# Optimization experiments

Hardware: AMD Instinct MI355X
Metric: run time of the kernel (lower is better)

The kernel has to match this reference:

```python
import jax, jax.numpy as jnp
import numpy as np

TOP_K = 2  # router top-k (assumed, standard MoE)


def setup_inputs() -> dict:
    key = jax.random.key(0)
    ks = jax.random.split(key, 8)
    B, T, C, H, E = 4, 1024, 1024, 4096, 8
    s = 0.02
    return {
        "X": jax.random.normal(ks[0], (B, T, C), jnp.float32),
        "router_w": jax.random.normal(ks[1], (C, E), jnp.float32) * s,
        "sh_w1": jax.random.normal(ks[2], (C, H), jnp.float32) * s,
        "sh_b1": jnp.zeros((H,), jnp.float32),
        "sh_w2": jax.random.normal(ks[3], (H, C), jnp.float32) * s,
        "sh_b2": jnp.zeros((C,), jnp.float32),
        "rt_w1": jax.random.normal(ks[4], (E, C, H), jnp.float32) * s,
        "rt_b1": jnp.zeros((E, H), jnp.float32),
        "rt_w2": jax.random.normal(ks[5], (E, H, C), jnp.float32) * s,
        "rt_b2": jnp.zeros((E, C), jnp.float32),
    }


def reference(X, router_w, sh_w1, sh_b1, sh_w2, sh_b2, rt_w1, rt_b1, rt_w2, rt_b2):
    B, T, C = X.shape
    E = router_w.shape[1]

    # --- router: softmax over experts, top-k weights/indices ---
    logits = jnp.einsum("btc,ce->bte", X, router_w)
    probs = jax.nn.softmax(logits, axis=-1)                 # [B,T,E]
    weights, indices = jax.lax.top_k(probs, TOP_K)          # [B,T,K]

    # --- aux load-balance loss: E * sum_i f_i * P_i ---
    onehot = jax.nn.one_hot(indices, E, dtype=X.dtype)      # [B,T,K,E]
    f = onehot.sum(axis=2).mean(axis=(0, 1))                # fraction of tokens per expert
    P = probs.mean(axis=(0, 1))                             # mean router prob per expert
    aux_loss = E * jnp.sum(f * P)

    # --- shared expert(s): single MLP (num_shared_experts = 1) ---
    shared = jnp.einsum("bth,hc->btc", jax.nn.relu(jnp.einsum("btc,ch->bth", X, sh_w1) + sh_b1), sh_w2) + sh_b2

    # --- routed experts: dense all-expert MLP, then weighted combine ---
    h = jax.nn.relu(jnp.einsum("btc,ech->bteh", X, rt_w1) + rt_b1)        # [B,T,E,H]
    y = jnp.einsum("bteh,ehc->btec", h, rt_w2) + rt_b2                    # [B,T,E,C]
    w_full = jnp.einsum("btk,btke->bte", weights, onehot)                 # per-token expert weight
    routed = jnp.einsum("bte,btec->btc", w_full, y)

    return shared + routed, aux_loss
```

## Files before the change

### kernel.cpp

```cpp
#include <hip/hip_runtime.h>


typedef unsigned short u16;
typedef __bf16 bf16x8 __attribute__((ext_vector_type(8)));
typedef float f32x4 __attribute__((ext_vector_type(4)));

#define NTOK 4096
#define CDIM 1024
#define HDIM 4096
#define NEXP 8
#define SLOTS 14336
#define NTILES 56
#define RBLK 1024

#define WAITVM(N) do { asm volatile("s_waitcnt vmcnt(" #N ")" ::: "memory"); } while (0)

static __device__ __forceinline__ u16 f2bf(float f) {
  unsigned u = __float_as_uint(f);
  u += 0x7fffu + ((u >> 16) & 1u);
  return (u16)(u >> 16);
}

static __device__ __forceinline__ void gload16(const void* g, void* l) {
  __builtin_amdgcn_global_load_lds((const __attribute__((address_space(1))) unsigned int*)g,
                                   (__attribute__((address_space(3))) unsigned int*)l,
                                   16, 0, 0);
}

__global__ void init_kernel(int* order, int* tile_expert, int* cursor) {
  int i = blockIdx.x * 256 + threadIdx.x;
  if (i < SLOTS) order[i] = (i < NTOK) ? i : -1;
  if (i < NTILES) tile_expert[i] = (i < 16) ? 8 : -1;
  if (i < NEXP) cursor[i] = 0;
}

__global__ void xconv_kernel(const float* __restrict__ X, u16* __restrict__ Xb) {
  int i = blockIdx.x * 256 + threadIdx.x;
  float4 v = ((const float4*)X)[i];
  u16 o0 = f2bf(v.x), o1 = f2bf(v.y), o2 = f2bf(v.z), o3 = f2bf(v.w);
  unsigned long long pack = (unsigned long long)o0 | ((unsigned long long)o1 << 16)
                          | ((unsigned long long)o2 << 32) | ((unsigned long long)o3 << 48);
  ((unsigned long long*)Xb)[i] = pack;
}

__global__ void tconv_kernel(const float* __restrict__ src, u16* __restrict__ dst, int R, int Cc) {
  __shared__ float t[32][33];
  const size_t bofs = (size_t)blockIdx.z * R * Cc;
  src += bofs; dst += bofs;
  int tx = threadIdx.x & 31, ty = threadIdx.x >> 5;
  int r0 = blockIdx.y * 32, c0 = blockIdx.x * 32;
#pragma unroll
  for (int i = 0; i < 32; i += 8)
    t[ty + i][tx] = src[(size_t)(r0 + ty + i) * Cc + c0 + tx];
  __syncthreads();
#pragma unroll
  for (int i = 0; i < 32; i += 8)
    dst[(size_t)(c0 + ty + i) * R + r0 + tx] = f2bf(t[tx][ty + i]);
}

__global__ __launch_bounds__(256) void router_kernel(
    const float* __restrict__ X, const float* __restrict__ rw,
    float* __restrict__ w01, int* __restrict__ e01,
    float* __restrict__ pP, int* __restrict__ pC) {
  __shared__ float wP[4][8];
  __shared__ int wE[4][2];
  const int tid = threadIdx.x;
  const int w = tid >> 6, l = tid & 63;
  const int wid = blockIdx.x * 4 + w;
  const float* x = X + (size_t)wid * CDIM;
  float s[8] = {0.f,0.f,0.f,0.f,0.f,0.f,0.f,0.f};
#pragma unroll 4
  for (int i = 0; i < 16; ++i) {
    int c = i * 64 + l;
    float xv = x[c];
    const float4* rp = (const float4*)(rw + c * 8);
    float4 r0 = rp[0], r1 = rp[1];
    s[0] += xv * r0.x; s[1] += xv * r0.y; s[2] += xv * r0.z; s[3] += xv * r0.w;
    s[4] += xv * r1.x; s[5] += xv * r1.y; s[6] += xv * r1.z; s[7] += xv * r1.w;
  }
#pragma unroll
  for (int off = 32; off; off >>= 1)
#pragma unroll
    for (int e = 0; e < 8; ++e) s[e] += __shfl_down(s[e], off);
  if (l == 0) {
    float m = s[0];
#pragma unroll
    for (int e = 1; e < 8; ++e) m = fmaxf(m, s[e]);
    float p[8], d = 0.f;
#pragma unroll
    for (int e = 0; e < 8; ++e) { p[e] = expf(s[e] - m); d += p[e]; }
    float inv = 1.f / d;
#pragma unroll
    for (int e = 0; e < 8; ++e) p[e] *= inv;
    int e0 = 0;
#pragma unroll
    for (int e = 1; e < 8; ++e) if (p[e] > p[e0]) e0 = e;
    int e1 = -1;
#pragma unroll
    for (int e = 0; e < 8; ++e) if (e != e0 && (e1 < 0 || p[e] > p[e1])) e1 = e;
    w01[wid * 2] = p[e0]; w01[wid * 2 + 1] = p[e1];
    e01[wid * 2] = e0;    e01[wid * 2 + 1] = e1;
#pragma unroll
    for (int e = 0; e < 8; ++e) wP[w][e] = p[e];
    wE[w][0] = e0; wE[w][1] = e1;
  }
  __syncthreads();
  if (tid < 8) {
    pP[blockIdx.x * 8 + tid] = wP[0][tid] + wP[1][tid] + wP[2][tid] + wP[3][tid];
    int c = 0;
#pragma unroll
    for (int v = 0; v < 4; ++v) c += (wE[v][0] == tid) + (wE[v][1] == tid);
    pC[blockIdx.x * 8 + tid] = c;
  }
}

__global__ __launch_bounds__(256) void setup_kernel(
    const float* __restrict__ pP, const int* __restrict__ pC,
    int* __restrict__ roff, int* __restrict__ tile_expert, float* __restrict__ out_aux) {
  __shared__ float sP[32][8];
  __shared__ int   sC[32][8];
  const int tid = threadIdx.x;
  const int e = tid & 7, g = tid >> 3;
  float fs = 0.f; int cs = 0;
  for (int b = g; b < RBLK; b += 32) { fs += pP[b * 8 + e]; cs += pC[b * 8 + e]; }
  sP[g][e] = fs; sC[g][e] = cs;
  __syncthreads();
  if (tid == 0) {
    float P[8]; int C[8];
    for (int e2 = 0; e2 < 8; ++e2) {
      float f2 = 0.f; int c2 = 0;
      for (int g2 = 0; g2 < 32; ++g2) { f2 += sP[g2][e2]; c2 += sC[g2][e2]; }
      P[e2] = f2; C[e2] = c2;
    }
    int off = NTOK;
    float a = 0.f;
    for (int e2 = 0; e2 < NEXP; ++e2) {
      roff[e2] = off;
      int nt = (C[e2] + 255) >> 8;
      int t0 = off >> 8;
      for (int i = 0; i < nt; ++i) tile_expert[t0 + i] = e2;
      off += nt << 8;
      a += (C[e2] * (1.f / NTOK)) * (P[e2] * (1.f / NTOK));
    }
    out_aux[0] = (float)NEXP * a;
  }
}

__global__ __launch_bounds__(256) void scatter_kernel(
    const int* __restrict__ e01, const int* __restrict__ roff,
    int* __restrict__ cursor, int* __restrict__ order, int* __restrict__ slot_of) {
  __shared__ int cnt_l[8];
  __shared__ int base_l[8];
  const int tid = threadIdx.x;
  const int t = blockIdx.x * 256 + tid;
  if (tid < 8) cnt_l[tid] = 0;
  __syncthreads();
  int e0 = e01[t * 2], e1 = e01[t * 2 + 1];
  int p0 = atomicAdd(&cnt_l[e0], 1);
  int p1 = atomicAdd(&cnt_l[e1], 1);
  __syncthreads();
  if (tid < 8) base_l[tid] = atomicAdd(&cursor[tid], cnt_l[tid]);
  __syncthreads();
  int s0 = roff[e0] + base_l[e0] + p0;
  int s1 = roff[e1] + base_l[e1] + p1;
  order[s0] = t; order[s1] = t;
  slot_of[t * 2] = s0; slot_of[t * 2 + 1] = s1;
}


__global__ __launch_bounds__(512, 2) void gemm_h_kernel(
    const u16* __restrict__ Xb, const u16* __restrict__ W1t, const u16* __restrict__ RW1t,
    const float* __restrict__ sh_b1, const float* __restrict__ rt_b1,
    const int* __restrict__ tile_expert, const int* __restrict__ order,
    u16* __restrict__ Hu) {
  const int orig = blockIdx.y * 16 + blockIdx.x;
  const int wg = (orig & 7) * 112 + (orig >> 3);
  const int tile = wg >> 4, nidx = wg & 15;
  int e = tile_expert[tile];
  if (e < 0) return;
  const u16* Bw = (e == 8) ? W1t : RW1t + (size_t)e * HDIM * CDIM;
  const float* bias = (e == 8) ? sh_b1 : rt_b1 + e * HDIM;

  __shared__ u16 LDS[65536];
  u16* As = LDS;
  u16* Bs = LDS + 32768;

  const int tid = threadIdx.x;
  const int l = tid & 63, w = tid >> 6;
  const int wm = w >> 2, wn = w & 3;
  const int fr = l & 15, fq = l >> 4;
  const int m0 = tile * 256, n0 = nidx * 256;

  int tok0 = order[m0 + 32 * w + fr];      if (tok0 < 0) tok0 = 0;
  int tok1 = order[m0 + 32 * w + 16 + fr]; if (tok1 < 0) tok1 = 0;
  const u16* aSrc0 = Xb + (size_t)tok0 * CDIM + fq * 8;
  const u16* aSrc1 = Xb + (size_t)tok1 * CDIM + fq * 8;
  const u16* bSrc0 = Bw + (size_t)(n0 + 32 * w + fr) * CDIM + fq * 8;
  const u16* bSrc1 = Bw + (size_t)(n0 + 32 * w + 16 + fr) * CDIM + fq * 8;

  auto STAGE_A = [&](int bi, int kofs) {
    gload16(aSrc0 + kofs, As + bi * 8192 + (2 * w + 0) * 512);
    gload16(aSrc1 + kofs, As + bi * 8192 + (2 * w + 1) * 512);
  };
  auto STAGE_B = [&](int bi, int kofs) {
    gload16(bSrc0 + kofs, Bs + bi * 8192 + (2 * w + 0) * 512);
    gload16(bSrc1 + kofs, Bs + bi * 8192 + (2 * w + 1) * 512);
  };

  float bvf[4];
#pragma unroll
  for (int j = 0; j < 4; ++j) bvf[j] = bias[n0 + wn * 64 + j * 16 + fr];

  f32x4 acc[8][4] = {};
  const int NT = CDIM / 32;
  STAGE_A(0, 0); STAGE_B(0, 0); STAGE_A(1, 32); STAGE_B(1, 32);

#pragma unroll 1
  for (int t = 0; t < NT; ++t) {
    const int bi = t & 3, pf = (t + 2) & 3, kof = (t + 2) * 32;
    if (t < NT - 1) { WAITVM(4); } else { WAITVM(0); }
    __builtin_amdgcn_s_barrier();
    __builtin_amdgcn_sched_barrier(0);
    const u16* ab = As + bi * 8192 + l * 8;
    const u16* bb = Bs + bi * 8192 + l * 8;
    if (t + 2 < NT) STAGE_A(pf, kof);
    bf16x8 av[4], bv[4];
#pragma unroll
    for (int j = 0; j < 4; ++j) bv[j] = *(const bf16x8*)&bb[(wn * 4 + j) * 512];
#pragma unroll
    for (int i = 0; i < 4; ++i) av[i] = *(const bf16x8*)&ab[(wm * 8 + i) * 512];
    __builtin_amdgcn_s_setprio(1);
#pragma unroll
    for (int i = 0; i < 4; ++i)
#pragma unroll
      for (int j = 0; j < 4; ++j)
        acc[i][j] = __builtin_amdgcn_mfma_f32_16x16x32_bf16(av[i], bv[j], acc[i][j], 0, 0, 0);
    __builtin_amdgcn_s_setprio(0);
    if (t + 2 < NT) STAGE_B(pf, kof);
    bf16x8 aw[4];
#pragma unroll
    for (int i = 0; i < 4; ++i) aw[i] = *(const bf16x8*)&ab[(wm * 8 + 4 + i) * 512];
    __builtin_amdgcn_s_setprio(1);
#pragma unroll
    for (int i = 0; i < 4; ++i)
#pragma unroll
      for (int j = 0; j < 4; ++j)
        acc[4 + i][j] = __builtin_amdgcn_mfma_f32_16x16x32_bf16(aw[i], bv[j], acc[4 + i][j], 0, 0, 0);
    __builtin_amdgcn_s_setprio(0);
  }

  for (int half = 0; half < 2; ++half) {
    __syncthreads();
    if (wm == half) {
#pragma unroll
      for (int i = 0; i < 8; ++i)
#pragma unroll
        for (int j = 0; j < 4; ++j) {
          const int col = wn * 64 + j * 16 + fr;
#pragma unroll
          for (int r = 0; r < 4; ++r) {
            float v = fmaxf(acc[i][j][r] + bvf[j], 0.0f);
            LDS[(i * 16 + fq * 4 + r) * 264 + col] = f2bf(v);
          }
        }
    }
    __syncthreads();
#pragma unroll
    for (int ps = 0; ps < 8; ++ps) {
      int idx = ps * 512 + tid, row = idx >> 5, c = idx & 31;
      bf16x8 vv = *(const bf16x8*)&LDS[row * 264 + c * 8];
      *(bf16x8*)&Hu[(size_t)(m0 + half * 128 + row) * HDIM + n0 + c * 8] = vv;
    }
  }
}

__global__ __launch_bounds__(512, 2) void gemm_o_kernel(
    const u16* __restrict__ Hu, const u16* __restrict__ W2t, const u16* __restrict__ RW2t,
    const float* __restrict__ sh_b2, const float* __restrict__ rt_b2,
    const int* __restrict__ tile_expert,
    float* __restrict__ Yu) {
  const int orig = blockIdx.y * 4 + blockIdx.x;
  const int wg = (orig & 7) * 28 + (orig >> 3);
  const int tile = wg >> 2, nidx = wg & 3;
  int e = tile_expert[tile];
  if (e < 0) return;
  const u16* Bw = (e == 8) ? W2t : RW2t + (size_t)e * CDIM * HDIM;
  const float* bias = (e == 8) ? sh_b2 : rt_b2 + e * CDIM;

  __shared__ u16 LDS2[65536];
  u16* As = LDS2;
  u16* Bs = LDS2 + 32768;

  const int tid = threadIdx.x;
  const int l = tid & 63, w = tid >> 6;
  const int wm = w >> 2, wn = w & 3;
  const int fr = l & 15, fq = l >> 4;
  const int m0 = tile * 256, n0 = nidx * 256;

  const u16* aSrc0 = Hu + (size_t)(m0 + 32 * w + fr) * HDIM + fq * 8;
  const u16* aSrc1 = Hu + (size_t)(m0 + 32 * w + 16 + fr) * HDIM + fq * 8;
  const u16* bSrc0 = Bw + (size_t)(n0 + 32 * w + fr) * HDIM + fq * 8;
  const u16* bSrc1 = Bw + (size_t)(n0 + 32 * w + 16 + fr) * HDIM + fq * 8;

  auto STAGE_A = [&](int bi, int kofs) {
    gload16(aSrc0 + kofs, As + bi * 8192 + (2 * w + 0) * 512);
    gload16(aSrc1 + kofs, As + bi * 8192 + (2 * w + 1) * 512);
  };
  auto STAGE_B = [&](int bi, int kofs) {
    gload16(bSrc0 + kofs, Bs + bi * 8192 + (2 * w + 0) * 512);
    gload16(bSrc1 + kofs, Bs + bi * 8192 + (2 * w + 1) * 512);
  };

  float bvf[4];
#pragma unroll
  for (int j = 0; j < 4; ++j) bvf[j] = bias[n0 + wn * 64 + j * 16 + fr];

  f32x4 acc[8][4] = {};
  const int NT = HDIM / 32;
  STAGE_A(0, 0); STAGE_B(0, 0); STAGE_A(1, 32); STAGE_B(1, 32);

#pragma unroll 1
  for (int t = 0; t < NT; ++t) {
    const int bi = t & 3, pf = (t + 2) & 3, kof = (t + 2) * 32;
    if (t < NT - 1) { WAITVM(4); } else { WAITVM(0); }
    __builtin_amdgcn_s_barrier();
    __builtin_amdgcn_sched_barrier(0);
    const u16* ab = As + bi * 8192 + l * 8;
    const u16* bb = Bs + bi * 8192 + l * 8;
    if (t + 2 < NT) STAGE_A(pf, kof);
    bf16x8 av[4], bv[4];
#pragma unroll
    for (int j = 0; j < 4; ++j) bv[j] = *(const bf16x8*)&bb[(wn * 4 + j) * 512];
#pragma unroll
    for (int i = 0; i < 4; ++i) av[i] = *(const bf16x8*)&ab[(wm * 8 + i) * 512];
    __builtin_amdgcn_s_setprio(1);
#pragma unroll
    for (int i = 0; i < 4; ++i)
#pragma unroll
      for (int j = 0; j < 4; ++j)
        acc[i][j] = __builtin_amdgcn_mfma_f32_16x16x32_bf16(av[i], bv[j], acc[i][j], 0, 0, 0);
    __builtin_amdgcn_s_setprio(0);
    if (t + 2 < NT) STAGE_B(pf, kof);
    bf16x8 aw[4];
#pragma unroll
    for (int i = 0; i < 4; ++i) aw[i] = *(const bf16x8*)&ab[(wm * 8 + 4 + i) * 512];
    __builtin_amdgcn_s_setprio(1);
#pragma unroll
    for (int i = 0; i < 4; ++i)
#pragma unroll
      for (int j = 0; j < 4; ++j)
        acc[4 + i][j] = __builtin_amdgcn_mfma_f32_16x16x32_bf16(aw[i], bv[j], acc[4 + i][j], 0, 0, 0);
    __builtin_amdgcn_s_setprio(0);
  }

  const size_t mb = m0 + wm * 128;
#pragma unroll
  for (int j = 0; j < 4; ++j) {
    const int n_g = n0 + wn * 64 + j * 16 + fr;
#pragma unroll
    for (int i = 0; i < 8; ++i)
#pragma unroll
      for (int r = 0; r < 4; ++r)
        Yu[(mb + i * 16 + fq * 4 + r) * (size_t)CDIM + n_g] = acc[i][j][r] + bvf[j];
  }
}

__global__ void combine_kernel(const float* __restrict__ Yu, const float* __restrict__ w01,
                               const int* __restrict__ slot_of, float* __restrict__ out) {
  int gid = blockIdx.x * 256 + threadIdx.x;
  int t = gid >> 8;
  int c4 = gid & 255;
  int s0 = slot_of[t * 2], s1 = slot_of[t * 2 + 1];
  float wq0 = w01[t * 2], wq1 = w01[t * 2 + 1];
  float4 a  = ((const float4*)(Yu + (size_t)t  * CDIM))[c4];
  float4 b0 = ((const float4*)(Yu + (size_t)s0 * CDIM))[c4];
  float4 b1 = ((const float4*)(Yu + (size_t)s1 * CDIM))[c4];
  float4 rv;
  rv.x = a.x + wq0 * b0.x + wq1 * b1.x;
  rv.y = a.y + wq0 * b0.y + wq1 * b1.y;
  rv.z = a.z + wq0 * b0.z + wq1 * b1.z;
  rv.w = a.w + wq0 * b0.w + wq1 * b1.w;
  ((float4*)out)[gid] = rv;
}

extern "C" void kernel_launch(void* const* d_in, const int* in_sizes, int n_in,
                              void* d_out, int out_size, void* d_ws, size_t ws_size,
                              hipStream_t stream) {
  const float* X        = (const float*)d_in[0];
  const float* router_w = (const float*)d_in[1];
  const float* sh_w1    = (const float*)d_in[2];
  const float* sh_b1    = (const float*)d_in[3];
  const float* sh_w2    = (const float*)d_in[4];
  const float* sh_b2    = (const float*)d_in[5];
  const float* rt_w1    = (const float*)d_in[6];
  const float* rt_b1    = (const float*)d_in[7];
  const float* rt_w2    = (const float*)d_in[8];
  const float* rt_b2    = (const float*)d_in[9];
  float* out = (float*)d_out;

  char* p = (char*)d_ws;
  auto take = [&](size_t bytes) { char* q = p; p += (bytes + 255) & ~(size_t)255; return q; };
  u16*  Xb   = (u16*)take((size_t)NTOK * CDIM * 2);
  u16*  W1t  = (u16*)take((size_t)HDIM * CDIM * 2);
  u16*  W2t  = (u16*)take((size_t)CDIM * HDIM * 2);
  u16*  RW1t = (u16*)take((size_t)NEXP * HDIM * CDIM * 2);
  u16*  RW2t = (u16*)take((size_t)NEXP * CDIM * HDIM * 2);
  u16*  Hu   = (u16*)take((size_t)SLOTS * HDIM * 2);
  float* Yu  = (float*)take((size_t)SLOTS * CDIM * 4);
  float* w01 = (float*)take((size_t)NTOK * 2 * 4);
  int*  e01  = (int*)take((size_t)NTOK * 2 * 4);
  int*  slot_of = (int*)take((size_t)NTOK * 2 * 4);
  int*  order   = (int*)take((size_t)SLOTS * 4);
  int*  tile_expert = (int*)take((size_t)NTILES * 4);
  float* pP  = (float*)take((size_t)RBLK * 8 * 4);
  int*  pC   = (int*)take((size_t)RBLK * 8 * 4);
  int*  cursor = (int*)take(256);
  int*  roff   = (int*)take(256);
  size_t need = (size_t)(p - (char*)d_ws);
  if (ws_size < need) return;

  init_kernel<<<NTILES, 256, 0, stream>>>(order, tile_expert, cursor);
  xconv_kernel<<<(NTOK * CDIM / 4) / 256, 256, 0, stream>>>(X, Xb);
  tconv_kernel<<<dim3(HDIM / 32, CDIM / 32, 1), 256, 0, stream>>>(sh_w1, W1t, CDIM, HDIM);
  tconv_kernel<<<dim3(CDIM / 32, HDIM / 32, 1), 256, 0, stream>>>(sh_w2, W2t, HDIM, CDIM);
  tconv_kernel<<<dim3(HDIM / 32, CDIM / 32, NEXP), 256, 0, stream>>>(rt_w1, RW1t, CDIM, HDIM);
  tconv_kernel<<<dim3(CDIM / 32, HDIM / 32, NEXP), 256, 0, stream>>>(rt_w2, RW2t, HDIM, CDIM);
  router_kernel<<<RBLK, 256, 0, stream>>>(X, router_w, w01, e01, pP, pC);
  setup_kernel<<<1, 256, 0, stream>>>(pP, pC, roff, tile_expert, out + (size_t)NTOK * CDIM);
  scatter_kernel<<<NTOK / 256, 256, 0, stream>>>(e01, roff, cursor, order, slot_of);
  gemm_h_kernel<<<dim3(16, NTILES), 512, 0, stream>>>(
      Xb, W1t, RW1t, sh_b1, rt_b1, tile_expert, order, Hu);
  gemm_o_kernel<<<dim3(4, NTILES), 512, 0, stream>>>(
      Hu, W2t, RW2t, sh_b2, rt_b2, tile_expert, Yu);
  combine_kernel<<<(NTOK * CDIM / 4) / 256, 256, 0, stream>>>(Yu, w01, slot_of, out);
}
```

Before: 441.9 us.

## Fuse fp32 weight transpose and bf16 conversion into GEMM B-operand loading

Removes the four separate transpose-and-convert kernels that rewrote all shared and routed weights to bf16 in a transposed layout before every call. Each GEMM now loads fp32 weights directly through registers, converts them to bf16 and writes them to LDS in the MFMA fragment layout. This uses double-buffered B, triple-buffered A and a reworked wait/barrier schedule. It avoids a large extra read/write pass over the weights, but the GEMMs now read twice as many weight bytes (fp32) and do per-tile conversion work. Each GEMM tile re-reads and re-converts the weights, including tiles for the same expert.

```diff
diff --git a/kernel.cpp b/kernel.cpp
--- a/kernel.cpp
+++ b/kernel.cpp
@@ -4,6 +4,7 @@
 typedef unsigned short u16;
 typedef __bf16 bf16x8 __attribute__((ext_vector_type(8)));
 typedef float f32x4 __attribute__((ext_vector_type(4)));
+typedef u16 u16x8 __attribute__((ext_vector_type(8)));
 
 #define NTOK 4096
 #define CDIM 1024
@@ -14,6 +15,7 @@
 #define RBLK 1024
 
 #define WAITVM(N) do { asm volatile("s_waitcnt vmcnt(" #N ")" ::: "memory"); } while (0)
+#define WAITLGKM do { asm volatile("s_waitcnt lgkmcnt(0)" ::: "memory"); } while (0)
 
 static __device__ __forceinline__ u16 f2bf(float f) {
   unsigned u = __float_as_uint(f);
@@ -41,21 +43,6 @@
   unsigned long long pack = (unsigned long long)o0 | ((unsigned long long)o1 << 16)
                           | ((unsigned long long)o2 << 32) | ((unsigned long long)o3 << 48);
   ((unsigned long long*)Xb)[i] = pack;
-}
-
-__global__ void tconv_kernel(const float* __restrict__ src, u16* __restrict__ dst, int R, int Cc) {
-  __shared__ float t[32][33];
-  const size_t bofs = (size_t)blockIdx.z * R * Cc;
-  src += bofs; dst += bofs;
-  int tx = threadIdx.x & 31, ty = threadIdx.x >> 5;
-  int r0 = blockIdx.y * 32, c0 = blockIdx.x * 32;
-#pragma unroll
-  for (int i = 0; i < 32; i += 8)
-    t[ty + i][tx] = src[(size_t)(r0 + ty + i) * Cc + c0 + tx];
-  __syncthreads();
-#pragma unroll
-  for (int i = 0; i < 32; i += 8)
-    dst[(size_t)(c0 + ty + i) * R + r0 + tx] = f2bf(t[tx][ty + i]);
 }
 
 __global__ __launch_bounds__(256) void router_kernel(
@@ -169,7 +156,7 @@
 
 
 __global__ __launch_bounds__(512, 2) void gemm_h_kernel(
-    const u16* __restrict__ Xb, const u16* __restrict__ W1t, const u16* __restrict__ RW1t,
+    const u16* __restrict__ Xb, const float* __restrict__ W1, const float* __restrict__ RW1,
     const float* __restrict__ sh_b1, const float* __restrict__ rt_b1,
     const int* __restrict__ tile_expert, const int* __restrict__ order,
     u16* __restrict__ Hu) {
@@ -178,12 +165,12 @@
   const int tile = wg >> 4, nidx = wg & 15;
   int e = tile_expert[tile];
   if (e < 0) return;
-  const u16* Bw = (e == 8) ? W1t : RW1t + (size_t)e * HDIM * CDIM;
+  const float* Bw = (e == 8) ? W1 : RW1 + (size_t)e * CDIM * HDIM;
   const float* bias = (e == 8) ? sh_b1 : rt_b1 + e * HDIM;
 
-  __shared__ u16 LDS[65536];
+  __shared__ u16 LDS[40960];
   u16* As = LDS;
-  u16* Bs = LDS + 32768;
+  u16* Bs = LDS + 24576;
 
   const int tid = threadIdx.x;
   const int l = tid & 63, w = tid >> 6;
@@ -195,16 +182,25 @@
   int tok1 = order[m0 + 32 * w + 16 + fr]; if (tok1 < 0) tok1 = 0;
   const u16* aSrc0 = Xb + (size_t)tok0 * CDIM + fq * 8;
   const u16* aSrc1 = Xb + (size_t)tok1 * CDIM + fq * 8;
-  const u16* bSrc0 = Bw + (size_t)(n0 + 32 * w + fr) * CDIM + fq * 8;
-  const u16* bSrc1 = Bw + (size_t)(n0 + 32 * w + 16 + fr) * CDIM + fq * 8;
-
   auto STAGE_A = [&](int bi, int kofs) {
     gload16(aSrc0 + kofs, As + bi * 8192 + (2 * w + 0) * 512);
     gload16(aSrc1 + kofs, As + bi * 8192 + (2 * w + 1) * 512);
   };
-  auto STAGE_B = [&](int bi, int kofs) {
-    gload16(bSrc0 + kofs, Bs + bi * 8192 + (2 * w + 0) * 512);
-    gload16(bSrc1 + kofs, Bs + bi * 8192 + (2 * w + 1) * 512);
+
+  const float* bSrc = Bw + (size_t)((l >> 5) * 16) * HDIM + (n0 + 32 * w + (l & 31));
+  float bq[16];
+  auto LOAD_B = [&](int kt) {
+    const float* s = bSrc + (size_t)kt * 32 * HDIM;
+#pragma unroll
+    for (int j = 0; j < 16; ++j) bq[j] = s[(size_t)j * HDIM];
+  };
+  u16* bBase = Bs + (2 * w + ((l & 31) >> 4)) * 512 + (l & 15) * 8 + (l >> 5) * 256;
+  auto WRITE_B = [&](int bi) {
+    u16x8 v0, v1;
+#pragma unroll
+    for (int j = 0; j < 8; ++j) { v0[j] = f2bf(bq[j]); v1[j] = f2bf(bq[8 + j]); }
+    *(u16x8*)(bBase + bi * 8192) = v0;
+    *(u16x8*)(bBase + bi * 8192 + 128) = v1;
   };
 
   float bvf[4];
@@ -213,40 +209,47 @@
 
   f32x4 acc[8][4] = {};
   const int NT = CDIM / 32;
-  STAGE_A(0, 0); STAGE_B(0, 0); STAGE_A(1, 32); STAGE_B(1, 32);
+  STAGE_A(0, 0); STAGE_A(1, 32);
+  LOAD_B(0);
+  WAITVM(0);
+  WRITE_B(0);
+  LOAD_B(1);
+  WAITLGKM;
+  __builtin_amdgcn_s_barrier();
+  __builtin_amdgcn_sched_barrier(0);
 
 #pragma unroll 1
   for (int t = 0; t < NT; ++t) {
-    const int bi = t & 3, pf = (t + 2) & 3, kof = (t + 2) * 32;
-    if (t < NT - 1) { WAITVM(4); } else { WAITVM(0); }
-    __builtin_amdgcn_s_barrier();
-    __builtin_amdgcn_sched_barrier(0);
-    const u16* ab = As + bi * 8192 + l * 8;
-    const u16* bb = Bs + bi * 8192 + l * 8;
-    if (t + 2 < NT) STAGE_A(pf, kof);
-    bf16x8 av[4], bv[4];
+    if (t + 2 < NT) STAGE_A((t + 2) % 3, (t + 2) * 32);
+    const u16* ab = As + (t % 3) * 8192 + l * 8;
+    const u16* bb = Bs + (t & 1) * 8192 + l * 8;
+    bf16x8 av[4], bv[4], aw[4];
 #pragma unroll
     for (int j = 0; j < 4; ++j) bv[j] = *(const bf16x8*)&bb[(wn * 4 + j) * 512];
 #pragma unroll
     for (int i = 0; i < 4; ++i) av[i] = *(const bf16x8*)&ab[(wm * 8 + i) * 512];
+#pragma unroll
+    for (int i = 0; i < 4; ++i) aw[i] = *(const bf16x8*)&ab[(wm * 8 + 4 + i) * 512];
     __builtin_amdgcn_s_setprio(1);
 #pragma unroll
     for (int i = 0; i < 4; ++i)
 #pragma unroll
       for (int j = 0; j < 4; ++j)
         acc[i][j] = __builtin_amdgcn_mfma_f32_16x16x32_bf16(av[i], bv[j], acc[i][j], 0, 0, 0);
-    __builtin_amdgcn_s_setprio(0);
-    if (t + 2 < NT) STAGE_B(pf, kof);
-    bf16x8 aw[4];
-#pragma unroll
-    for (int i = 0; i < 4; ++i) aw[i] = *(const bf16x8*)&ab[(wm * 8 + 4 + i) * 512];
-    __builtin_amdgcn_s_setprio(1);
 #pragma unroll
     for (int i = 0; i < 4; ++i)
 #pragma unroll
       for (int j = 0; j < 4; ++j)
         acc[4 + i][j] = __builtin_amdgcn_mfma_f32_16x16x32_bf16(aw[i], bv[j], acc[4 + i][j], 0, 0, 0);
     __builtin_amdgcn_s_setprio(0);
+    if (t + 1 < NT) {
+      if (t + 2 < NT) { WAITVM(2); } else { WAITVM(0); }
+      WRITE_B((t + 1) & 1);
+      if (t + 2 < NT) LOAD_B(t + 2);
+      WAITLGKM;
+      __builtin_amdgcn_s_barrier();
+      __builtin_amdgcn_sched_barrier(0);
+    }
   }
 
   for (int half = 0; half < 2; ++half) {
@@ -268,14 +271,14 @@
 #pragma unroll
     for (int ps = 0; ps < 8; ++ps) {
       int idx = ps * 512 + tid, row = idx >> 5, c = idx & 31;
-      bf16x8 vv = *(const bf16x8*)&LDS[row * 264 + c * 8];
-      *(bf16x8*)&Hu[(size_t)(m0 + half * 128 + row) * HDIM + n0 + c * 8] = vv;
+      u16x8 vv = *(const u16x8*)&LDS[row * 264 + c * 8];
+      *(u16x8*)&Hu[(size_t)(m0 + half * 128 + row) * HDIM + n0 + c * 8] = vv;
     }
   }
 }
 
 __global__ __launch_bounds__(512, 2) void gemm_o_kernel(
-    const u16* __restrict__ Hu, const u16* __restrict__ W2t, const u16* __restrict__ RW2t,
+    const u16* __restrict__ Hu, const float* __restrict__ W2, const float* __restrict__ RW2,
     const float* __restrict__ sh_b2, const float* __restrict__ rt_b2,
     const int* __restrict__ tile_expert,
     float* __restrict__ Yu) {
@@ -284,12 +287,12 @@
   const int tile = wg >> 2, nidx = wg & 3;
   int e = tile_expert[tile];
   if (e < 0) return;
-  const u16* Bw = (e == 8) ? W2t : RW2t + (size_t)e * CDIM * HDIM;
+  const float* Bw = (e == 8) ? W2 : RW2 + (size_t)e * HDIM * CDIM;
   const float* bias = (e == 8) ? sh_b2 : rt_b2 + e * CDIM;
 
-  __shared__ u16 LDS2[65536];
+  __shared__ u16 LDS2[40960];
   u16* As = LDS2;
-  u16* Bs = LDS2 + 32768;
+  u16* Bs = LDS2 + 24576;
 
   const int tid = threadIdx.x;
   const int l = tid & 63, w = tid >> 6;
@@ -299,16 +302,25 @@
 
   const u16* aSrc0 = Hu + (size_t)(m0 + 32 * w + fr) * HDIM + fq * 8;
   const u16* aSrc1 = Hu + (size_t)(m0 + 32 * w + 16 + fr) * HDIM + fq * 8;
-  const u16* bSrc0 = Bw + (size_t)(n0 + 32 * w + fr) * HDIM + fq * 8;
-  const u16* bSrc1 = Bw + (size_t)(n0 + 32 * w + 16 + fr) * HDIM + fq * 8;
-
   auto STAGE_A = [&](int bi, int kofs) {
     gload16(aSrc0 + kofs, As + bi * 8192 + (2 * w + 0) * 512);
     gload16(aSrc1 + kofs, As + bi * 8192 + (2 * w + 1) * 512);
   };
-  auto STAGE_B = [&](int bi, int kofs) {
-    gload16(bSrc0 + kofs, Bs + bi * 8192 + (2 * w + 0) * 512);
-    gload16(bSrc1 + kofs, Bs + bi * 8192 + (2 * w + 1) * 512);
+
+  const float* bSrc = Bw + (size_t)((l >> 5) * 16) * CDIM + (n0 + 32 * w + (l & 31));
+  float bq[16];
+  auto LOAD_B = [&](int kt) {
+    const float* s = bSrc + (size_t)kt * 32 * CDIM;
+#pragma unroll
+    for (int j = 0; j < 16; ++j) bq[j] = s[(size_t)j * CDIM];
+  };
+  u16* bBase = Bs + (2 * w + ((l & 31) >> 4)) * 512 + (l & 15) * 8 + (l >> 5) * 256;
+  auto WRITE_B = [&](int bi) {
+    u16x8 v0, v1;
+#pragma unroll
+    for (int j = 0; j < 8; ++j) { v0[j] = f2bf(bq[j]); v1[j] = f2bf(bq[8 + j]); }
+    *(u16x8*)(bBase + bi * 8192) = v0;
+    *(u16x8*)(bBase + bi * 8192 + 128) = v1;
   };
 
   float bvf[4];
@@ -317,40 +329,47 @@
 
   f32x4 acc[8][4] = {};
   const int NT = HDIM / 32;
-  STAGE_A(0, 0); STAGE_B(0, 0); STAGE_A(1, 32); STAGE_B(1, 32);
+  STAGE_A(0, 0); STAGE_A(1, 32);
+  LOAD_B(0);
+  WAITVM(0);
+  WRITE_B(0);
+  LOAD_B(1);
+  WAITLGKM;
+  __builtin_amdgcn_s_barrier();
+  __builtin_amdgcn_sched_barrier(0);
 
 #pragma unroll 1
   for (int t = 0; t < NT; ++t) {
-    const int bi = t & 3, pf = (t + 2) & 3, kof = (t + 2) * 32;
-    if (t < NT - 1) { WAITVM(4); } else { WAITVM(0); }
-    __builtin_amdgcn_s_barrier();
-    __builtin_amdgcn_sched_barrier(0);
-    const u16* ab = As + bi * 8192 + l * 8;
-    const u16* bb = Bs + bi * 8192 + l * 8;
-    if (t + 2 < NT) STAGE_A(pf, kof);
-    bf16x8 av[4], bv[4];
+    if (t + 2 < NT) STAGE_A((t + 2) % 3, (t + 2) * 32);
+    const u16* ab = As + (t % 3) * 8192 + l * 8;
+    const u16* bb = Bs + (t & 1) * 8192 + l * 8;
+    bf16x8 av[4], bv[4], aw[4];
 #pragma unroll
     for (int j = 0; j < 4; ++j) bv[j] = *(const bf16x8*)&bb[(wn * 4 + j) * 512];
 #pragma unroll
     for (int i = 0; i < 4; ++i) av[i] = *(const bf16x8*)&ab[(wm * 8 + i) * 512];
+#pragma unroll
+    for (int i = 0; i < 4; ++i) aw[i] = *(const bf16x8*)&ab[(wm * 8 + 4 + i) * 512];
     __builtin_amdgcn_s_setprio(1);
 #pragma unroll
     for (int i = 0; i < 4; ++i)
 #pragma unroll
       for (int j = 0; j < 4; ++j)
         acc[i][j] = __builtin_amdgcn_mfma_f32_16x16x32_bf16(av[i], bv[j], acc[i][j], 0, 0, 0);
-    __builtin_amdgcn_s_setprio(0);
-    if (t + 2 < NT) STAGE_B(pf, kof);
-    bf16x8 aw[4];
-#pragma unroll
-    for (int i = 0; i < 4; ++i) aw[i] = *(const bf16x8*)&ab[(wm * 8 + 4 + i) * 512];
-    __builtin_amdgcn_s_setprio(1);
 #pragma unroll
     for (int i = 0; i < 4; ++i)
 #pragma unroll
       for (int j = 0; j < 4; ++j)
         acc[4 + i][j] = __builtin_amdgcn_mfma_f32_16x16x32_bf16(aw[i], bv[j], acc[4 + i][j], 0, 0, 0);
     __builtin_amdgcn_s_setprio(0);
+    if (t + 1 < NT) {
+      if (t + 2 < NT) { WAITVM(2); } else { WAITVM(0); }
+      WRITE_B((t + 1) & 1);
+      if (t + 2 < NT) LOAD_B(t + 2);
+      WAITLGKM;
+      __builtin_amdgcn_s_barrier();
+      __builtin_amdgcn_sched_barrier(0);
+    }
   }
 
   const size_t mb = m0 + wm * 128;
@@ -401,10 +420,6 @@
   char* p = (char*)d_ws;
   auto take = [&](size_t bytes) { char* q = p; p += (bytes + 255) & ~(size_t)255; return q; };
   u16*  Xb   = (u16*)take((size_t)NTOK * CDIM * 2);
-  u16*  W1t  = (u16*)take((size_t)HDIM * CDIM * 2);
-  u16*  W2t  = (u16*)take((size_t)CDIM * HDIM * 2);
-  u16*  RW1t = (u16*)take((size_t)NEXP * HDIM * CDIM * 2);
-  u16*  RW2t = (u16*)take((size_t)NEXP * CDIM * HDIM * 2);
   u16*  Hu   = (u16*)take((size_t)SLOTS * HDIM * 2);
   float* Yu  = (float*)take((size_t)SLOTS * CDIM * 4);
   float* w01 = (float*)take((size_t)NTOK * 2 * 4);
@@ -421,16 +436,12 @@
 
   init_kernel<<<NTILES, 256, 0, stream>>>(order, tile_expert, cursor);
   xconv_kernel<<<(NTOK * CDIM / 4) / 256, 256, 0, stream>>>(X, Xb);
-  tconv_kernel<<<dim3(HDIM / 32, CDIM / 32, 1), 256, 0, stream>>>(sh_w1, W1t, CDIM, HDIM);
-  tconv_kernel<<<dim3(CDIM / 32, HDIM / 32, 1), 256, 0, stream>>>(sh_w2, W2t, HDIM, CDIM);
-  tconv_kernel<<<dim3(HDIM / 32, CDIM / 32, NEXP), 256, 0, stream>>>(rt_w1, RW1t, CDIM, HDIM);
-  tconv_kernel<<<dim3(CDIM / 32, HDIM / 32, NEXP), 256, 0, stream>>>(rt_w2, RW2t, HDIM, CDIM);
   router_kernel<<<RBLK, 256, 0, stream>>>(X, router_w, w01, e01, pP, pC);
   setup_kernel<<<1, 256, 0, stream>>>(pP, pC, roff, tile_expert, out + (size_t)NTOK * CDIM);
   scatter_kernel<<<NTOK / 256, 256, 0, stream>>>(e01, roff, cursor, order, slot_of);
   gemm_h_kernel<<<dim3(16, NTILES), 512, 0, stream>>>(
-      Xb, W1t, RW1t, sh_b1, rt_b1, tile_expert, order, Hu);
+      Xb, sh_w1, rt_w1, sh_b1, rt_b1, tile_expert, order, Hu);
   gemm_o_kernel<<<dim3(4, NTILES), 512, 0, stream>>>(
-      Hu, W2t, RW2t, sh_b2, rt_b2, tile_expert, Yu);
+      Hu, sh_w2, rt_w2, sh_b2, rt_b2, tile_expert, Yu);
   combine_kernel<<<(NTOK * CDIM / 4) / 256, 256, 0, stream>>>(Yu, w01, slot_of, out);
 }
```

After: 422.4 us. 4.4% less time.
